# Kernel optimization log

Measured on AMD Instinct MI355X. Metric: run time of the kernel, lower is better.

## Reference

```python
import jax, jax.numpy as jnp
import numpy as np

TOP_K = 2  # config.num_active_experts


def setup_inputs() -> dict:
    key = jax.random.key(0)
    k1, k2, k3, k4 = jax.random.split(key, 4)
    B, S, D = 2, 2048, 1024
    E, W = 8, 1024  # 8 experts, each width 1024 -> total_expert_width = 8192
    x = jax.random.normal(k1, (B, S, D), dtype=jnp.float32)
    router_w = jax.random.normal(k2, (E, D), dtype=jnp.float32) * 0.02
    w1 = jax.random.normal(k3, (D, E * W), dtype=jnp.float32) * 0.02
    w2 = jax.random.normal(k4, (E * W, D), dtype=jnp.float32) * 0.02
    return {"x": x, "router_w": router_w, "w1": w1, "w2": w2}


def reference(x, router_w, w1, w2):
    B, S, D = x.shape
    E = router_w.shape[0]
    W = w1.shape[1] // E  # uniform expert width
    T = B * S
    xf = x.reshape(T, D)

    # Router: sigmoid gating, top-k, sum-normalized weights (norm_topk_prob)
    router_logits = jnp.einsum('td,ed->te', xf, router_w)
    router_probs = jax.nn.sigmoid(router_logits.astype(jnp.float32))
    top_w, sel = jax.lax.top_k(router_probs, TOP_K)          # [T,K]
    top_w = top_w / (top_w.sum(axis=-1, keepdims=True) + 1e-20)
    top_w = top_w.astype(x.dtype)

    # Expert MLPs: expert e uses w1[:, off_e:off_e+W], w2[off_e:off_e+W, :].
    # Uniform width -> single batched einsum over experts (same math as the
    # padded-gather / block-sparse SDD/DSD grouped GEMM pipeline).
    W1e = w1.reshape(D, E, W).transpose(1, 0, 2)             # [E,D,W]
    W2e = w2.reshape(E, W, D)                                # [E,W,D]
    h = jnp.einsum('td,edw->etw', xf, W1e)                   # up-proj
    a = jnp.square(jax.nn.relu(h))                           # relu_squared
    y = jnp.einsum('etw,ewd->etd', a, W2e)                   # down-proj

    # Weighted scatter-combine: combine_weights[t,e] = top_w if e selected else 0
    cw = jnp.zeros((T, E), dtype=x.dtype).at[jnp.arange(T)[:, None], sel].set(top_w)
    out = jnp.einsum('etd,te->td', y, cw)
    return out.reshape(B, S, D)
```

## Files before the change

kernel.cpp:

```cpp
#include <hip/hip_runtime.h>
#include <hip/hip_bf16.h>


#define T_TOKENS 4096
#define DD 1024
#define EE 8
#define WW 1024
#define CAP 1536
#define BM 128
#define BN 128
#define BK 64
#define MT (CAP / BM)
#define NT (WW / BN)
#define GEMM_BLOCKS (EE * MT * NT)
#define TR1_BLOCKS 512
#define TR2_BLOCKS 512
#define TLD 132

typedef short bf16x8 __attribute__((ext_vector_type(8)));
typedef float f32x4 __attribute__((ext_vector_type(4)));

__device__ __forceinline__ void gload_lds16(const void* g, void* l) {
  __builtin_amdgcn_global_load_lds((__attribute__((address_space(1))) void*)(g),
                                   (__attribute__((address_space(3))) void*)(l),
                                   16, 0, 0);
}

__device__ __forceinline__ float bf2f(unsigned short u) {
  union { unsigned int i; float f; } v; v.i = (unsigned int)u << 16; return v.f;
}

__device__ __forceinline__ unsigned short f2bf_u(float f) {
  __hip_bfloat16 h = __float2bfloat16(f);
  union { __hip_bfloat16 h; unsigned short u; } c; c.h = h; return c.u;
}

__device__ __forceinline__ void transpose_tile_128(
    const float* __restrict__ src, long src_ld, long r0, long c0,
    unsigned short* __restrict__ dst, long dst_ld, unsigned short* lds)
{
  int tid = threadIdx.x;
  int cq = tid & 31;
  int rb = tid >> 5;
#pragma unroll
  for (int i = 0; i < 16; i++) {
    int r = rb + i * 8;
    f32x4 v = *(const f32x4*)(src + (r0 + r) * src_ld + c0 + cq * 4);
#pragma unroll
    for (int j = 0; j < 4; j++)
      lds[(cq * 4 + j) * TLD + r] = f2bf_u(v[j]);
  }
  __syncthreads();
#pragma unroll
  for (int it = 0; it < 8; it++) {
    int slot = it * 256 + tid;
    int c = slot >> 4;
    int m = slot & 15;
    const unsigned short* p = lds + (size_t)c * TLD + m * 8;
    uint2 lo = *(const uint2*)(p);
    uint2 hi = *(const uint2*)(p + 4);
    uint4 o; o.x = lo.x; o.y = lo.y; o.z = hi.x; o.w = hi.y;
    *(uint4*)(dst + (c0 + c) * dst_ld + r0 + m * 8) = o;
  }
}

__global__ __launch_bounds__(256) void pre_kernel(
    const float* __restrict__ w1, const float* __restrict__ x,
    const float* __restrict__ rw,
    __hip_bfloat16* __restrict__ w1t, __hip_bfloat16* __restrict__ xb,
    int* __restrict__ sel, float* __restrict__ wpair)
{
  __shared__ unsigned short lds_t[128 * TLD];
  int b = blockIdx.x;
  if (b < TR1_BLOCKS) {
    int e = b & 7;
    int t = b >> 3;
    int bn = e * 8 + (t >> 3);
    int bd = t & 7;
    transpose_tile_128(w1, EE * WW, (long)bd * 128, (long)bn * 128,
                       (unsigned short*)w1t, DD, lds_t);
  } else {
    int lane = threadIdx.x & 63;
    int wave = threadIdx.x >> 6;
    int t = (b - TR1_BLOCKS) * 4 + wave;
    const float* xrow = x + (size_t)t * DD;
    float acc[EE];
#pragma unroll
    for (int e = 0; e < EE; e++) acc[e] = 0.f;
#pragma unroll
    for (int i = 0; i < DD / 64; i++) {
      int d = lane + i * 64;
      float xv = xrow[d];
      xb[t * DD + d] = __float2bfloat16(xv);
#pragma unroll
      for (int e = 0; e < EE; e++) acc[e] += xv * rw[e * DD + d];
    }
#pragma unroll
    for (int e = 0; e < EE; e++) {
#pragma unroll
      for (int off = 32; off > 0; off >>= 1)
        acc[e] += __shfl_down(acc[e], off, 64);
    }
    if (lane == 0) {
      float p[EE];
#pragma unroll
      for (int e = 0; e < EE; e++) p[e] = 1.f / (1.f + expf(-acc[e]));
      int e0 = 0; float b0 = p[0];
      for (int e = 1; e < EE; e++) if (p[e] > b0) { b0 = p[e]; e0 = e; }
      int e1 = -1; float b1 = -1.f;
      for (int e = 0; e < EE; e++) {
        if (e == e0) continue;
        if (p[e] > b1) { b1 = p[e]; e1 = e; }
      }
      float s = b0 + b1 + 1e-20f;
      sel[t] = e0 | (e1 << 8);
      wpair[2 * t]     = b0 / s;
      wpair[2 * t + 1] = b1 / s;
    }
  }
}

__global__ __launch_bounds__(1024) void build_lists(
    const int* __restrict__ sel, int* __restrict__ counts,
    int* __restrict__ idx, int* __restrict__ tslot)
{
  __shared__ int lcnt[EE];
  int tid = threadIdx.x, lane = tid & 63;
  if (tid < EE) lcnt[tid] = 0;
  __syncthreads();
  unsigned long long lower = (1ull << lane) - 1;
#pragma unroll
  for (int j = 0; j < T_TOKENS / 1024; j++) {
    int t = j * 1024 + tid;
    int s = sel[t];
    int e0 = s & 0xff, e1 = (s >> 8) & 0xff;
    int slot0 = 0, slot1 = 0;
#pragma unroll
    for (int e = 0; e < EE; e++) {
      unsigned long long m0 = __ballot(e0 == e);
      unsigned long long m1 = __ballot(e1 == e);
      int c0 = __popcll(m0), c1 = __popcll(m1);
      int base = 0;
      if (lane == 0 && (c0 + c1) > 0) base = atomicAdd(&lcnt[e], c0 + c1);
      base = __shfl(base, 0, 64);
      if (e0 == e) slot0 = base + __popcll(m0 & lower);
      if (e1 == e) slot1 = base + c0 + __popcll(m1 & lower);
    }
    int p0 = e0 * CAP + slot0, p1 = e1 * CAP + slot1;
    idx[p0] = t; idx[p1] = t;
    tslot[2 * t] = p0; tslot[2 * t + 1] = p1;
  }
  __syncthreads();
  if (tid < EE) counts[tid] = lcnt[tid];
}

__global__ __launch_bounds__(256, 3) void gemm1_kernel(
    const __hip_bfloat16* __restrict__ xb, const __hip_bfloat16* __restrict__ w1t,
    const int* __restrict__ counts, const int* __restrict__ idx,
    __hip_bfloat16* __restrict__ act,
    const float* __restrict__ w2, __hip_bfloat16* __restrict__ w2t)
{
  __shared__ __attribute__((aligned(16))) char smem[128 * TLD * 2];
  int bid = blockIdx.x;
  if (bid < TR2_BLOCKS) {
    int e = bid & 7;
    int t2 = bid >> 3;
    transpose_tile_128(w2 + (long)e * WW * DD, DD,
                       (long)(t2 >> 3) * 128, (long)(t2 & 7) * 128,
                       (unsigned short*)(w2t + (long)e * DD * WW), WW,
                       (unsigned short*)smem);
    return;
  }
  short* As = (short*)smem;
  short* Bs = (short*)(smem + 16384);
  int g = bid - TR2_BLOCKS;
  int e = g & 7;
  int i = g >> 3;
  int mt = i >> 3, nt = i & 7;
  int n_e = counts[e];
  if (mt * BM >= n_e) return;

  int tid = threadIdx.x;
  int lane = tid & 63;
  int wave = __builtin_amdgcn_readfirstlane(tid >> 6);
  int wm = (wave >> 1) * 64, wn = (wave & 1) * 64;
  int m16 = lane & 15, qd = lane >> 4;

  const __hip_bfloat16* gA[4];
  const __hip_bfloat16* gB[4];
#pragma unroll
  for (int i2 = 0; i2 < 4; i2++) {
    int s = i2 * 256 + tid;
    int r = s >> 3;
    int q = (s & 7) ^ (r & 7);
    int rowA = mt * BM + r;
    int slot = rowA < n_e ? rowA : n_e - 1;
    int tok = idx[e * CAP + slot];
    gA[i2] = xb + (size_t)tok * DD + q * 8;
    gB[i2] = w1t + ((size_t)e * WW + nt * BN + r) * DD + q * 8;
  }
  short* ldsA[4];
  short* ldsB[4];
#pragma unroll
  for (int i2 = 0; i2 < 4; i2++) {
    ldsA[i2] = As + (i2 * 256 + wave * 64) * 8;
    ldsB[i2] = Bs + (i2 * 256 + wave * 64) * 8;
  }

  int aoff[4][2], boff[4][2];
#pragma unroll
  for (int mi = 0; mi < 4; mi++) {
    int r = wm + mi * 16 + m16;
#pragma unroll
    for (int h = 0; h < 2; h++)
      aoff[mi][h] = (r * 8 + ((qd + h * 4) ^ (r & 7))) * 8;
  }
#pragma unroll
  for (int ni = 0; ni < 4; ni++) {
    int r = wn + ni * 16 + m16;
#pragma unroll
    for (int h = 0; h < 2; h++)
      boff[ni][h] = (r * 8 + ((qd + h * 4) ^ (r & 7))) * 8;
  }

  f32x4 zero = {0.f, 0.f, 0.f, 0.f};
  f32x4 acc[4][4];
#pragma unroll
  for (int mi = 0; mi < 4; mi++)
#pragma unroll
    for (int ni = 0; ni < 4; ni++) acc[mi][ni] = zero;

  for (int k0 = 0; k0 < DD; k0 += BK) {
#pragma unroll
    for (int i2 = 0; i2 < 4; i2++) gload_lds16(gA[i2] + k0, ldsA[i2]);
#pragma unroll
    for (int i2 = 0; i2 < 4; i2++) gload_lds16(gB[i2] + k0, ldsB[i2]);
    __syncthreads();
#pragma unroll
    for (int h = 0; h < 2; h++) {
      bf16x8 af[4], bfr[4];
#pragma unroll
      for (int mi = 0; mi < 4; mi++) af[mi] = *(const bf16x8*)(As + aoff[mi][h]);
#pragma unroll
      for (int ni = 0; ni < 4; ni++) bfr[ni] = *(const bf16x8*)(Bs + boff[ni][h]);
#pragma unroll
      for (int mi = 0; mi < 4; mi++)
#pragma unroll
        for (int ni = 0; ni < 4; ni++)
          acc[mi][ni] = __builtin_amdgcn_mfma_f32_16x16x32_bf16(
              af[mi], bfr[ni], acc[mi][ni], 0, 0, 0);
    }
    __syncthreads();
  }

#pragma unroll
  for (int mi = 0; mi < 4; mi++) {
#pragma unroll
    for (int reg = 0; reg < 4; reg++) {
      int rowt = mt * BM + wm + mi * 16 + qd * 4 + reg;
      if (rowt < n_e) {
#pragma unroll
        for (int ni = 0; ni < 4; ni++) {
          float v = acc[mi][ni][reg];
          v = v > 0.f ? v * v : 0.f;
          int col = nt * BN + wn + ni * 16 + m16;
          act[((size_t)e * CAP + rowt) * WW + col] = __float2bfloat16(v);
        }
      }
    }
  }
}

__global__ __launch_bounds__(256, 3) void gemm2_kernel(
    const __hip_bfloat16* __restrict__ act, const __hip_bfloat16* __restrict__ w2t,
    const int* __restrict__ counts, __hip_bfloat16* __restrict__ y)
{
  __shared__ __attribute__((aligned(16))) char smem[32768];
  short* As = (short*)smem;
  short* Bs = (short*)(smem + 16384);
  int bid = blockIdx.x;
  int e = bid & 7;
  int i = bid >> 3;
  int mt = i >> 3, nt = i & 7;
  int n_e = counts[e];
  if (mt * BM >= n_e) return;

  int tid = threadIdx.x;
  int lane = tid & 63;
  int wave = __builtin_amdgcn_readfirstlane(tid >> 6);
  int wm = (wave >> 1) * 64, wn = (wave & 1) * 64;
  int m16 = lane & 15, qd = lane >> 4;

  const __hip_bfloat16* gA[4];
  const __hip_bfloat16* gB[4];
#pragma unroll
  for (int i2 = 0; i2 < 4; i2++) {
    int s = i2 * 256 + tid;
    int r = s >> 3;
    int q = (s & 7) ^ (r & 7);
    gA[i2] = act + ((size_t)e * CAP + mt * BM + r) * WW + q * 8;
    gB[i2] = w2t + ((size_t)e * DD + nt * BN + r) * WW + q * 8;
  }
  short* ldsA[4];
  short* ldsB[4];
#pragma unroll
  for (int i2 = 0; i2 < 4; i2++) {
    ldsA[i2] = As + (i2 * 256 + wave * 64) * 8;
    ldsB[i2] = Bs + (i2 * 256 + wave * 64) * 8;
  }

  int aoff[4][2], boff[4][2];
#pragma unroll
  for (int mi = 0; mi < 4; mi++) {
    int r = wm + mi * 16 + m16;
#pragma unroll
    for (int h = 0; h < 2; h++)
      aoff[mi][h] = (r * 8 + ((qd + h * 4) ^ (r & 7))) * 8;
  }
#pragma unroll
  for (int ni = 0; ni < 4; ni++) {
    int r = wn + ni * 16 + m16;
#pragma unroll
    for (int h = 0; h < 2; h++)
      boff[ni][h] = (r * 8 + ((qd + h * 4) ^ (r & 7))) * 8;
  }

  f32x4 zero = {0.f, 0.f, 0.f, 0.f};
  f32x4 acc[4][4];
#pragma unroll
  for (int mi = 0; mi < 4; mi++)
#pragma unroll
    for (int ni = 0; ni < 4; ni++) acc[mi][ni] = zero;

  for (int k0 = 0; k0 < WW; k0 += BK) {
#pragma unroll
    for (int i2 = 0; i2 < 4; i2++) gload_lds16(gA[i2] + k0, ldsA[i2]);
#pragma unroll
    for (int i2 = 0; i2 < 4; i2++) gload_lds16(gB[i2] + k0, ldsB[i2]);
    __syncthreads();
#pragma unroll
    for (int h = 0; h < 2; h++) {
      bf16x8 af[4], bfr[4];
#pragma unroll
      for (int mi = 0; mi < 4; mi++) af[mi] = *(const bf16x8*)(As + aoff[mi][h]);
#pragma unroll
      for (int ni = 0; ni < 4; ni++) bfr[ni] = *(const bf16x8*)(Bs + boff[ni][h]);
#pragma unroll
      for (int mi = 0; mi < 4; mi++)
#pragma unroll
        for (int ni = 0; ni < 4; ni++)
          acc[mi][ni] = __builtin_amdgcn_mfma_f32_16x16x32_bf16(
              af[mi], bfr[ni], acc[mi][ni], 0, 0, 0);
    }
    __syncthreads();
  }

#pragma unroll
  for (int mi = 0; mi < 4; mi++) {
#pragma unroll
    for (int reg = 0; reg < 4; reg++) {
      int slot = mt * BM + wm + mi * 16 + qd * 4 + reg;
      if (slot < n_e) {
#pragma unroll
        for (int ni = 0; ni < 4; ni++) {
          int col = nt * BN + wn + ni * 16 + m16;
          y[((size_t)e * CAP + slot) * DD + col] = __float2bfloat16(acc[mi][ni][reg]);
        }
      }
    }
  }
}

__global__ __launch_bounds__(256) void combine_kernel(
    const __hip_bfloat16* __restrict__ y, const int* __restrict__ tslot,
    const float* __restrict__ wpair, float* __restrict__ out)
{
  int t = blockIdx.x;
  int c = threadIdx.x * 4;
  int s0 = tslot[2 * t], s1 = tslot[2 * t + 1];
  float w0 = wpair[2 * t], w1 = wpair[2 * t + 1];
  const unsigned short* yu = (const unsigned short*)y;
  ushort4 a = *(const ushort4*)(yu + (size_t)s0 * DD + c);
  ushort4 bq = *(const ushort4*)(yu + (size_t)s1 * DD + c);
  f32x4 o;
  o[0] = w0 * bf2f(a.x) + w1 * bf2f(bq.x);
  o[1] = w0 * bf2f(a.y) + w1 * bf2f(bq.y);
  o[2] = w0 * bf2f(a.z) + w1 * bf2f(bq.z);
  o[3] = w0 * bf2f(a.w) + w1 * bf2f(bq.w);
  *(f32x4*)(out + (size_t)t * DD + c) = o;
}

extern "C" void kernel_launch(void* const* d_in, const int* in_sizes, int n_in,
                              void* d_out, int out_size, void* d_ws, size_t ws_size,
                              hipStream_t stream)
{
  const float* x  = (const float*)d_in[0];
  const float* rw = (const float*)d_in[1];
  const float* w1 = (const float*)d_in[2];
  const float* w2 = (const float*)d_in[3];
  float* out = (float*)d_out;

  char* ws = (char*)d_ws;
  __hip_bfloat16* xb  = (__hip_bfloat16*)ws;  ws += (size_t)T_TOKENS * DD * 2;
  __hip_bfloat16* w1t = (__hip_bfloat16*)ws;  ws += (size_t)EE * WW * DD * 2;
  __hip_bfloat16* w2t = (__hip_bfloat16*)ws;  ws += (size_t)EE * DD * WW * 2;
  __hip_bfloat16* act = (__hip_bfloat16*)ws;  ws += (size_t)EE * CAP * WW * 2;
  __hip_bfloat16* y   = (__hip_bfloat16*)ws;  ws += (size_t)EE * CAP * DD * 2;
  int*   counts = (int*)ws;                   ws += 256;
  int*   idx    = (int*)ws;                   ws += (size_t)EE * CAP * 4;
  int*   sel    = (int*)ws;                   ws += (size_t)T_TOKENS * 4;
  int*   tslot  = (int*)ws;                   ws += (size_t)T_TOKENS * 8;
  float* wpair  = (float*)ws;                 ws += (size_t)T_TOKENS * 8;

  pre_kernel<<<TR1_BLOCKS + T_TOKENS / 4, 256, 0, stream>>>(
      w1, x, rw, w1t, xb, sel, wpair);
  build_lists<<<1, 1024, 0, stream>>>(sel, counts, idx, tslot);
  gemm1_kernel<<<TR2_BLOCKS + GEMM_BLOCKS, 256, 0, stream>>>(
      xb, w1t, counts, idx, act, w2, w2t);
  gemm2_kernel<<<GEMM_BLOCKS, 256, 0, stream>>>(act, w2t, counts, y);
  combine_kernel<<<T_TOKENS, 256, 0, stream>>>(y, tslot, wpair, out);
}
```

Before: 190.1 us.

## Move W2 transpose into list-building kernel and grid-stride combine

The W2 fp32-to-bf16 transpose now runs in 512 extra 1024-thread blocks of the single-block list-building kernel, instead of as prefix blocks of gemm1. This lets the transpose overlap with the serial routing-list construction rather than delay the GEMM blocks, and it shrinks gemm1's launch and shared memory. The combine kernel also switches to a grid-stride loop over 512 blocks. In exchange, the transpose uses a new 1024-thread tile mapping, and the combine launch exposes less parallelism.

Result: no change. 189.7 us (-0.2%).

```diff
diff --git a/kernel.cpp b/kernel.cpp
--- a/kernel.cpp
+++ b/kernel.cpp
@@ -14,7 +14,6 @@
 #define NT (WW / BN)
 #define GEMM_BLOCKS (EE * MT * NT)
 #define TR1_BLOCKS 512
-#define TR2_BLOCKS 512
 #define TLD 132
 
 typedef short bf16x8 __attribute__((ext_vector_type(8)));
@@ -120,62 +119,86 @@
   }
 }
 
-__global__ __launch_bounds__(1024) void build_lists(
+__global__ __launch_bounds__(1024) void lists_w2t_kernel(
     const int* __restrict__ sel, int* __restrict__ counts,
-    int* __restrict__ idx, int* __restrict__ tslot)
-{
+    int* __restrict__ idx, int* __restrict__ tslot,
+    const float* __restrict__ w2, __hip_bfloat16* __restrict__ w2t)
+{
+  __shared__ __attribute__((aligned(16))) unsigned short lds_t[128 * TLD];
   __shared__ int lcnt[EE];
-  int tid = threadIdx.x, lane = tid & 63;
-  if (tid < EE) lcnt[tid] = 0;
-  __syncthreads();
-  unsigned long long lower = (1ull << lane) - 1;
-#pragma unroll
-  for (int j = 0; j < T_TOKENS / 1024; j++) {
-    int t = j * 1024 + tid;
-    int s = sel[t];
-    int e0 = s & 0xff, e1 = (s >> 8) & 0xff;
-    int slot0 = 0, slot1 = 0;
-#pragma unroll
-    for (int e = 0; e < EE; e++) {
-      unsigned long long m0 = __ballot(e0 == e);
-      unsigned long long m1 = __ballot(e1 == e);
-      int c0 = __popcll(m0), c1 = __popcll(m1);
-      int base = 0;
-      if (lane == 0 && (c0 + c1) > 0) base = atomicAdd(&lcnt[e], c0 + c1);
-      base = __shfl(base, 0, 64);
-      if (e0 == e) slot0 = base + __popcll(m0 & lower);
-      if (e1 == e) slot1 = base + c0 + __popcll(m1 & lower);
-    }
-    int p0 = e0 * CAP + slot0, p1 = e1 * CAP + slot1;
-    idx[p0] = t; idx[p1] = t;
-    tslot[2 * t] = p0; tslot[2 * t + 1] = p1;
-  }
-  __syncthreads();
-  if (tid < EE) counts[tid] = lcnt[tid];
+  int bid = blockIdx.x;
+  int tid = threadIdx.x;
+  if (bid == 0) {
+    int lane = tid & 63;
+    if (tid < EE) lcnt[tid] = 0;
+    __syncthreads();
+    unsigned long long lower = (1ull << lane) - 1;
+#pragma unroll
+    for (int j = 0; j < T_TOKENS / 1024; j++) {
+      int t = j * 1024 + tid;
+      int s = sel[t];
+      int e0 = s & 0xff, e1 = (s >> 8) & 0xff;
+      int slot0 = 0, slot1 = 0;
+#pragma unroll
+      for (int e = 0; e < EE; e++) {
+        unsigned long long m0 = __ballot(e0 == e);
+        unsigned long long m1 = __ballot(e1 == e);
+        int c0 = __popcll(m0), c1 = __popcll(m1);
+        int base = 0;
+        if (lane == 0 && (c0 + c1) > 0) base = atomicAdd(&lcnt[e], c0 + c1);
+        base = __shfl(base, 0, 64);
+        if (e0 == e) slot0 = base + __popcll(m0 & lower);
+        if (e1 == e) slot1 = base + c0 + __popcll(m1 & lower);
+      }
+      int p0 = e0 * CAP + slot0, p1 = e1 * CAP + slot1;
+      idx[p0] = t; idx[p1] = t;
+      tslot[2 * t] = p0; tslot[2 * t + 1] = p1;
+    }
+    __syncthreads();
+    if (tid < EE) counts[tid] = lcnt[tid];
+  } else {
+    int e = bid & 7;
+    int t2 = (bid - 1) >> 3;
+    const float* src = w2 + (long)e * WW * DD;
+    unsigned short* dst = (unsigned short*)(w2t + (long)e * DD * WW);
+    long r0 = (long)(t2 >> 3) * 128;
+    long c0 = (long)(t2 & 7) * 128;
+    int cq = tid & 31;
+    int row = tid >> 5;
+#pragma unroll
+    for (int i = 0; i < 4; i++) {
+      int r = row + i * 32;
+      f32x4 v = *(const f32x4*)(src + (r0 + r) * DD + c0 + cq * 4);
+#pragma unroll
+      for (int j = 0; j < 4; j++)
+        lds_t[(cq * 4 + j) * TLD + r] = f2bf_u(v[j]);
+    }
+    __syncthreads();
+#pragma unroll
+    for (int it = 0; it < 2; it++) {
+      int slot = it * 1024 + tid;
+      int c = slot >> 4;
+      int m = slot & 15;
+      const unsigned short* p = lds_t + (size_t)c * TLD + m * 8;
+      uint2 lo = *(const uint2*)(p);
+      uint2 hi = *(const uint2*)(p + 4);
+      uint4 o; o.x = lo.x; o.y = lo.y; o.z = hi.x; o.w = hi.y;
+      *(uint4*)(dst + (c0 + c) * WW + r0 + m * 8) = o;
+    }
+  }
 }
 
 __global__ __launch_bounds__(256, 3) void gemm1_kernel(
     const __hip_bfloat16* __restrict__ xb, const __hip_bfloat16* __restrict__ w1t,
     const int* __restrict__ counts, const int* __restrict__ idx,
-    __hip_bfloat16* __restrict__ act,
-    const float* __restrict__ w2, __hip_bfloat16* __restrict__ w2t)
-{
-  __shared__ __attribute__((aligned(16))) char smem[128 * TLD * 2];
-  int bid = blockIdx.x;
-  if (bid < TR2_BLOCKS) {
-    int e = bid & 7;
-    int t2 = bid >> 3;
-    transpose_tile_128(w2 + (long)e * WW * DD, DD,
-                       (long)(t2 >> 3) * 128, (long)(t2 & 7) * 128,
-                       (unsigned short*)(w2t + (long)e * DD * WW), WW,
-                       (unsigned short*)smem);
-    return;
-  }
+    __hip_bfloat16* __restrict__ act)
+{
+  __shared__ __attribute__((aligned(16))) char smem[32768];
   short* As = (short*)smem;
   short* Bs = (short*)(smem + 16384);
-  int g = bid - TR2_BLOCKS;
-  int e = g & 7;
-  int i = g >> 3;
+  int bid = blockIdx.x;
+  int e = bid & 7;
+  int i = bid >> 3;
   int mt = i >> 3, nt = i & 7;
   int n_e = counts[e];
   if (mt * BM >= n_e) return;
@@ -375,19 +398,20 @@
     const __hip_bfloat16* __restrict__ y, const int* __restrict__ tslot,
     const float* __restrict__ wpair, float* __restrict__ out)
 {
-  int t = blockIdx.x;
   int c = threadIdx.x * 4;
-  int s0 = tslot[2 * t], s1 = tslot[2 * t + 1];
-  float w0 = wpair[2 * t], w1 = wpair[2 * t + 1];
-  const unsigned short* yu = (const unsigned short*)y;
-  ushort4 a = *(const ushort4*)(yu + (size_t)s0 * DD + c);
-  ushort4 bq = *(const ushort4*)(yu + (size_t)s1 * DD + c);
-  f32x4 o;
-  o[0] = w0 * bf2f(a.x) + w1 * bf2f(bq.x);
-  o[1] = w0 * bf2f(a.y) + w1 * bf2f(bq.y);
-  o[2] = w0 * bf2f(a.z) + w1 * bf2f(bq.z);
-  o[3] = w0 * bf2f(a.w) + w1 * bf2f(bq.w);
-  *(f32x4*)(out + (size_t)t * DD + c) = o;
+  for (int t = blockIdx.x; t < T_TOKENS; t += 512) {
+    int s0 = tslot[2 * t], s1 = tslot[2 * t + 1];
+    float w0 = wpair[2 * t], w1 = wpair[2 * t + 1];
+    const unsigned short* yu = (const unsigned short*)y;
+    ushort4 a = *(const ushort4*)(yu + (size_t)s0 * DD + c);
+    ushort4 bq = *(const ushort4*)(yu + (size_t)s1 * DD + c);
+    f32x4 o;
+    o[0] = w0 * bf2f(a.x) + w1 * bf2f(bq.x);
+    o[1] = w0 * bf2f(a.y) + w1 * bf2f(bq.y);
+    o[2] = w0 * bf2f(a.z) + w1 * bf2f(bq.z);
+    o[3] = w0 * bf2f(a.w) + w1 * bf2f(bq.w);
+    *(f32x4*)(out + (size_t)t * DD + c) = o;
+  }
 }
 
 extern "C" void kernel_launch(void* const* d_in, const int* in_sizes, int n_in,
@@ -414,9 +438,8 @@
 
   pre_kernel<<<TR1_BLOCKS + T_TOKENS / 4, 256, 0, stream>>>(
       w1, x, rw, w1t, xb, sel, wpair);
-  build_lists<<<1, 1024, 0, stream>>>(sel, counts, idx, tslot);
-  gemm1_kernel<<<TR2_BLOCKS + GEMM_BLOCKS, 256, 0, stream>>>(
-      xb, w1t, counts, idx, act, w2, w2t);
+  lists_w2t_kernel<<<513, 1024, 0, stream>>>(sel, counts, idx, tslot, w2, w2t);
+  gemm1_kernel<<<GEMM_BLOCKS, 256, 0, stream>>>(xb, w1t, counts, idx, act);
   gemm2_kernel<<<GEMM_BLOCKS, 256, 0, stream>>>(act, w2t, counts, y);
-  combine_kernel<<<T_TOKENS, 256, 0, stream>>>(y, tslot, wpair, out);
-}
+  combine_kernel<<<512, 256, 0, stream>>>(y, tslot, wpair, out);
+}
```
